# Kernel tuning notes

Measured on AMD Instinct MI355X. Metric: run time of the kernel, lower is better.

Reference implementation:

```python
import jax, jax.numpy as jnp
import numpy as np

B, T, D, H, L = 16, 1024, 1024, 1024, 2


def setup_inputs() -> dict:
    key = jax.random.key(0)
    ks = jax.random.split(key, 7)
    s_ih = float(np.sqrt(6.0 / (4 * H + D)))  # xavier_uniform bound
    s_hh = float(np.sqrt(6.0 / (4 * H + H)))
    return {
        "x": jax.random.normal(ks[0], (B, T, D), dtype=jnp.float32),
        "w_ih0": jax.random.uniform(ks[1], (4 * H, D), jnp.float32, -s_ih, s_ih),
        "w_hh0": jax.random.uniform(ks[2], (4 * H, H), jnp.float32, -s_hh, s_hh),
        "b0": jnp.zeros((4 * H,), jnp.float32),
        "w_ih1": jax.random.uniform(ks[3], (4 * H, H), jnp.float32, -s_ih, s_ih),
        "w_hh1": jax.random.uniform(ks[4], (4 * H, H), jnp.float32, -s_hh, s_hh),
        "b1": jnp.zeros((4 * H,), jnp.float32),
    }


def _cell(x, h, c, w_ih, w_hh, b):
    # gates: [B, 4H]
    gates = x @ w_ih.T + h @ w_hh.T + b
    i, f, g, o = jnp.split(gates, 4, axis=1)
    i = jnp.exp(i)            # exponential input gate (xLSTM sLSTM)
    f = jnp.exp(f)            # exponential forget gate
    g = jnp.tanh(g)
    o = jax.nn.sigmoid(o)
    c = f * c + i * g
    h = o * jnp.tanh(c)
    return h, c


def reference(x, w_ih0, w_hh0, b0, w_ih1, w_hh1, b1):
    b = x.shape[0]
    zeros = jnp.zeros((b, H), x.dtype)
    init = (zeros, zeros, zeros, zeros)  # (h0, c0, h1, c1)

    def step(carry, xt):
        h0, c0, h1, c1 = carry
        h0, c0 = _cell(xt, h0, c0, w_ih0, w_hh0, b0)
        h1, c1 = _cell(h0, h1, c1, w_ih1, w_hh1, b1)
        return (h0, c0, h1, c1), h1

    carry, ys = jax.lax.scan(step, init, jnp.swapaxes(x, 0, 1))  # time-major scan
    out = jnp.swapaxes(ys, 0, 1)  # [B, T, H]
    h0, c0, h1, c1 = carry
    return out, h0, c0, h1, c1
```

## Files before the change

kernel.cpp:

```cpp
#include <hip/hip_runtime.h>
#include <math.h>

namespace {
constexpr int Bt   = 16;
constexpr int Tt   = 1024;
constexpr int Hd   = 1024;
constexpr int NT   = 512;
constexpr int UPB  = 8;
constexpr int NROW = 32;

typedef unsigned long long u64;

__device__ __forceinline__ float sanitize_c(float v) {
  return fminf(fmaxf(v, -3.0e38f), 3.0e38f);
}

template <int CTRL>
__device__ __forceinline__ float dpp_add(float v) {
  int x = __builtin_amdgcn_update_dpp(0, __float_as_int(v), CTRL, 0xF, 0xF, true);
  return v + __int_as_float(x);
}
__device__ __forceinline__ float red8(float v) {
  v = dpp_add<0xB1>(v);
  v = dpp_add<0x4E>(v);
  v = dpp_add<0x141>(v);
  return v;
}

__device__ __forceinline__ u64 ld_h64(const float* p) {
  return __hip_atomic_load((const u64*)p, __ATOMIC_RELAXED, __HIP_MEMORY_SCOPE_AGENT);
}
__device__ __forceinline__ void st_h32(float* p, float v) {
  __hip_atomic_store(p, v, __ATOMIC_RELAXED, __HIP_MEMORY_SCOPE_AGENT);
}
}

__global__ __launch_bounds__(NT)
__attribute__((amdgpu_waves_per_eu(2, 2)))
void slstm_persist(
    const float* __restrict__ x,
    const float* __restrict__ wih0, const float* __restrict__ whh0, const float* __restrict__ b0v,
    const float* __restrict__ wih1, const float* __restrict__ whh1, const float* __restrict__ b1v,
    float* __restrict__ out, float* __restrict__ ws)
{
  __shared__ __align__(16) float in0[Bt * Hd];
  __shared__ __align__(16) float in1[Bt * Hd];
  __shared__ __align__(16) float red[64 * 17 * 4];
  __shared__ float gatel[NROW * Bt];
  __shared__ float cst[UPB * Bt];
  __shared__ float biasl[NROW];

  const int tid  = threadIdx.x;
  const int bid  = blockIdx.x;
  const int w    = tid >> 6;
  const int lane = tid & 63;
  const int kslo = lane & 7;
  const int rg   = lane >> 3;
  const int ks   = w * 8 + kslo;
  const bool isB = ks >= 32;
  const int ksl  = ks & 31;
  const int cell = bid >> 7;
  const int blk  = bid & 127;
  const int ubase = blk * UPB;

  unsigned* flags = (unsigned*)ws;
  float* h0buf = ws + 1024;
  float* h1buf = h0buf + 3 * Bt * Hd;

  const float* wmat = (cell == 0) ? (isB ? whh0 : wih0) : (isB ? whh1 : wih1);
  const float* bv   = (cell == 0) ? b0v : b1v;

  const int ro0 = ((0 + kslo) & 7) * 16;
  const int ro1 = ((1 + kslo) & 7) * 16;
  const int ro2 = ((2 + kslo) & 7) * 16;
  const int ro3 = ((3 + kslo) & 7) * 16;
  const int ro4 = ((4 + kslo) & 7) * 16;
  const int ro5 = ((5 + kslo) & 7) * 16;
  const int ro6 = ((6 + kslo) & 7) * 16;
  const int ro7 = ((7 + kslo) & 7) * 16;

  float4 w00,w01,w02,w03,w04,w05,w06,w07;
  float4 w10,w11,w12,w13,w14,w15,w16,w17;
  float4 w20,w21,w22,w23,w24,w25,w26,w27;
  float4 w30,w31,w32,w33,w34,w35,w36,w37;
#define LDW(r) { \
    const int lr = rg * 4 + r; \
    const char* wb = (const char*)(wmat + (size_t)((lr >> 3) * Hd + ubase + (lr & 7)) * Hd + ksl * 32); \
    w##r##0 = *(const float4*)(wb + ro0); w##r##1 = *(const float4*)(wb + ro1); \
    w##r##2 = *(const float4*)(wb + ro2); w##r##3 = *(const float4*)(wb + ro3); \
    w##r##4 = *(const float4*)(wb + ro4); w##r##5 = *(const float4*)(wb + ro5); \
    w##r##6 = *(const float4*)(wb + ro6); w##r##7 = *(const float4*)(wb + ro7); }
  LDW(0) LDW(1) LDW(2) LDW(3)
#undef LDW

  if (tid < NROW) biasl[tid] = bv[(tid >> 3) * Hd + ubase + (tid & 7)];
  if (tid < UPB * Bt) cst[tid] = 0.f;

  if (cell == 0) {
    #pragma unroll
    for (int p = 0; p < 8; ++p) {
      const int e = p * 2048 + tid * 4;
      const int b = e >> 10, d = e & 1023;
      *(float4*)(in0 + e) = *(const float4*)(x + (size_t)b * (Tt * Hd) + d);
    }
  }
  __syncthreads();

#define STEPC(c) { const float4 v = *(const float4*)(pb + ro##c); \
        a0 = fmaf(v.x, w0##c.x, a0); a0 = fmaf(v.y, w0##c.y, a0); \
        a0 = fmaf(v.z, w0##c.z, a0); a0 = fmaf(v.w, w0##c.w, a0); \
        a1 = fmaf(v.x, w1##c.x, a1); a1 = fmaf(v.y, w1##c.y, a1); \
        a1 = fmaf(v.z, w1##c.z, a1); a1 = fmaf(v.w, w1##c.w, a1); \
        a2 = fmaf(v.x, w2##c.x, a2); a2 = fmaf(v.y, w2##c.y, a2); \
        a2 = fmaf(v.z, w2##c.z, a2); a2 = fmaf(v.w, w2##c.w, a2); \
        a3 = fmaf(v.x, w3##c.x, a3); a3 = fmaf(v.y, w3##c.y, a3); \
        a3 = fmaf(v.z, w3##c.z, a3); a3 = fmaf(v.w, w3##c.w, a3); }
#define MATMUL(INBUF) { \
    const float* myin = (INBUF) + ksl * 32; \
    _Pragma("unroll 2") \
    for (int b = 0; b < Bt; ++b) { \
      const char* pb = (const char*)(myin + b * Hd); \
      float a0 = 0.f, a1 = 0.f, a2 = 0.f, a3 = 0.f; \
      STEPC(0) STEPC(1) STEPC(2) STEPC(3) \
      STEPC(4) STEPC(5) STEPC(6) STEPC(7) \
      a0 = red8(a0); a1 = red8(a1); a2 = red8(a2); a3 = red8(a3); \
      if (kslo == 0) \
        *(float4*)&red[((w * 8 + rg) * 17 + b) * 4] = make_float4(a0, a1, a2, a3); \
    } }

  for (int k = 0; k <= Tt + 1; ++k) {
    const bool act = (cell == 0) ? (k < Tt) : (k >= 2);

    if (w < 4) {
      if (act) { MATMUL(in0) }
    } else {
      const unsigned tgt = (unsigned)k;
      const int f = tid - 256;
      while (__hip_atomic_load(&flags[f], __ATOMIC_RELAXED, __HIP_MEMORY_SCOPE_AGENT) < tgt)
        __builtin_amdgcn_s_sleep(1);
    }
    __syncthreads();

    if (w >= 4) {
      if (act) {
        const int s = tid - 256;
        if ((cell == 0 && k == 0) || (cell == 1 && k == 2)) {
          #pragma unroll
          for (int p = 0; p < 16; ++p)
            *(float4*)(in1 + p * 1024 + s * 4) = make_float4(0.f, 0.f, 0.f, 0.f);
        } else {
          const float* src = (cell == 0) ? (h0buf + ((k - 1) % 3) * (Bt * Hd))
                                         : (h1buf + ((k - 1) & 1) * (Bt * Hd));
          #pragma unroll
          for (int p = 0; p < 16; ++p) {
            const int e = p * 1024 + s * 4;
            u64 lo = ld_h64(src + e), hi = ld_h64(src + e + 2);
            ((u64*)(in1 + e))[0] = lo;
            ((u64*)(in1 + e))[1] = hi;
          }
        }
      }
    } else {
      const int s = tid;
      if (cell == 0) {
        if (k + 1 < Tt) {
          #pragma unroll
          for (int p = 0; p < 16; ++p) {
            const int e = p * 1024 + s * 4;
            const int b = e >> 10, d = e & 1023;
            *(float4*)(in0 + e) =
                *(const float4*)(x + (size_t)b * (Tt * Hd) + (size_t)(k + 1) * Hd + d);
          }
        }
      } else if (k >= 1 && k <= Tt) {
        const float* src = h0buf + ((k - 1) % 3) * (Bt * Hd);
        #pragma unroll 8
        for (int p = 0; p < 16; ++p) {
          const int e = p * 1024 + s * 4;
          u64 lo = ld_h64(src + e), hi = ld_h64(src + e + 2);
          ((u64*)(in0 + e))[0] = lo;
          ((u64*)(in0 + e))[1] = hi;
        }
      }
    }
    __syncthreads();

    float oh = 0.f, oc = 0.f;
    if (act) {
      if (w >= 4) { MATMUL(in1) }
      __syncthreads();

      {
        const int rg2 = tid >> 6, rem = tid & 63, b2 = rem >> 2, r2 = rem & 3;
        float sgm = 0.f;
        #pragma unroll
        for (int ww = 0; ww < 8; ++ww)
          sgm += red[((ww * 8 + rg2) * 17 + b2) * 4 + r2];
        const int lr = rg2 * 4 + r2;
        gatel[lr * Bt + b2] = sgm + biasl[lr];
      }
      __syncthreads();

      if (tid < UPB * Bt) {
        const int u = tid >> 4, b2 = tid & 15;
        const float gi = gatel[(0 * UPB + u) * Bt + b2];
        const float gf = gatel[(1 * UPB + u) * Bt + b2];
        const float gg = gatel[(2 * UPB + u) * Bt + b2];
        const float go = gatel[(3 * UPB + u) * Bt + b2];
        const float ig = expf(gi);
        const float fg = expf(gf);
        const float g_ = tanhf(gg);
        const float og = 1.f / (1.f + expf(-go));
        const float cn = fg * cst[tid] + ig * g_;
        cst[tid] = cn;
        const float h = og * tanhf(cn);
        oh = h; oc = cn;
        const int j = ubase + u;
        if (cell == 0) {
          st_h32(&h0buf[(k % 3) * (Bt * Hd) + b2 * Hd + j], h);
        } else {
          st_h32(&h1buf[(k & 1) * (Bt * Hd) + b2 * Hd + j], h);
        }
      }
    }

    asm volatile("s_waitcnt vmcnt(0)" ::: "memory");
    __syncthreads();
    if (tid == 0)
      __hip_atomic_store(&flags[bid], (unsigned)(k + 1), __ATOMIC_RELAXED, __HIP_MEMORY_SCOPE_AGENT);

    if (act && tid < UPB * Bt) {
      const int u = tid >> 4, b2 = tid & 15, j = ubase + u;
      const size_t fin = (size_t)Bt * Tt * Hd;
      if (cell == 0) {
        if (k == Tt - 1) {
          out[fin + b2 * Hd + j] = oh;
          out[fin + Bt * Hd + b2 * Hd + j] = sanitize_c(oc);
        }
      } else {
        const int t = k - 2;
        out[((size_t)b2 * Tt + t) * Hd + j] = oh;
        if (t == Tt - 1) {
          out[fin + 2 * Bt * Hd + b2 * Hd + j] = oh;
          out[fin + 3 * Bt * Hd + b2 * Hd + j] = sanitize_c(oc);
        }
      }
    }
  }
  asm volatile("s_waitcnt vmcnt(0)" ::: "memory");
#undef MATMUL
#undef STEPC
}

extern "C" void kernel_launch(void* const* d_in, const int* in_sizes, int n_in,
                              void* d_out, int out_size, void* d_ws, size_t ws_size,
                              hipStream_t stream) {
  (void)hipMemsetAsync(d_ws, 0, 4096, stream);

  const float* x    = (const float*)d_in[0];
  const float* wih0 = (const float*)d_in[1];
  const float* whh0 = (const float*)d_in[2];
  const float* b0   = (const float*)d_in[3];
  const float* wih1 = (const float*)d_in[4];
  const float* whh1 = (const float*)d_in[5];
  const float* b1   = (const float*)d_in[6];

  slstm_persist<<<256, NT, 0, stream>>>(x, wih0, whh0, b0, wih1, whh1, b1,
                                        (float*)d_out, (float*)d_ws);
}
```

Measured before the change: 16.88 ms.

## Relay hidden state through per-XCD L2 mirrors with cooperative copy and XCD barrier

Each block now copies a slice of the freshly published h0/h1 buffers into a mirror buffer, using its rank within its XCD, then joins a per-XCD counter barrier. After a buffer_inv, all threads load the full hidden state from the mirror with plain float4 loads instead of many agent-scope atomic loads. The goal is to replace cross-XCD coherent reads by every block with one cooperative cross-XCD fetch per XCD, then serve the rest from the local L2. It adds an extra barrier and spin loop per timestep, and assumes exactly 32 blocks per XCD with 128 arrivals.

Result: slower. 29.66 ms (+75.7%).

```diff
diff --git a/kernel.cpp b/kernel.cpp
--- a/kernel.cpp
+++ b/kernel.cpp
@@ -8,6 +8,7 @@
 constexpr int NT   = 512;
 constexpr int UPB  = 8;
 constexpr int NROW = 32;
+constexpr int BH   = Bt * Hd;
 
 typedef unsigned long long u64;
 
@@ -32,6 +33,16 @@
 }
 __device__ __forceinline__ void st_h32(float* p, float v) {
   __hip_atomic_store(p, v, __ATOMIC_RELAXED, __HIP_MEMORY_SCOPE_AGENT);
+}
+
+__device__ __forceinline__ unsigned l2_atomic_add_ret(unsigned* p, unsigned v) {
+  unsigned old;
+  asm volatile("global_atomic_add %0, %1, %2, off sc0\n\ts_waitcnt vmcnt(0)"
+               : "=v"(old) : "v"(p), "v"(v) : "memory");
+  return old;
+}
+__device__ __forceinline__ void l2_atomic_add(unsigned* p, unsigned v) {
+  asm volatile("global_atomic_add %0, %1, off" :: "v"(p), "v"(v) : "memory");
 }
 }
 
@@ -43,12 +54,14 @@
     const float* __restrict__ wih1, const float* __restrict__ whh1, const float* __restrict__ b1v,
     float* __restrict__ out, float* __restrict__ ws)
 {
-  __shared__ __align__(16) float in0[Bt * Hd];
-  __shared__ __align__(16) float in1[Bt * Hd];
+  __shared__ __align__(16) float in0[BH];
+  __shared__ __align__(16) float in1[BH];
   __shared__ __align__(16) float red[64 * 17 * 4];
   __shared__ float gatel[NROW * Bt];
   __shared__ float cst[UPB * Bt];
   __shared__ float biasl[NROW];
+  __shared__ int lds_rank;
+  __shared__ int relayflag;
 
   const int tid  = threadIdx.x;
   const int bid  = blockIdx.x;
@@ -64,8 +77,12 @@
   const int ubase = blk * UPB;
 
   unsigned* flags = (unsigned*)ws;
+  unsigned* elect = (unsigned*)ws + 256;
+  unsigned* done  = (unsigned*)ws + 264;
   float* h0buf = ws + 1024;
-  float* h1buf = h0buf + 3 * Bt * Hd;
+  float* h1buf = h0buf + 3 * BH;
+  float* mir0  = h0buf + 5 * BH;
+  float* mir1  = h0buf + 8 * BH;
 
   const float* wmat = (cell == 0) ? (isB ? whh0 : wih0) : (isB ? whh1 : wih1);
   const float* bv   = (cell == 0) ? b0v : b1v;
@@ -93,6 +110,11 @@
   LDW(0) LDW(1) LDW(2) LDW(3)
 #undef LDW
 
+  const unsigned xcd = __builtin_amdgcn_s_getreg((31u << 11) | 20u) & 7u;
+  if (tid == 0) {
+    relayflag = 0;
+    lds_rank = (int)(l2_atomic_add_ret(elect + xcd, 1u) & 31u);
+  }
   if (tid < NROW) biasl[tid] = bv[(tid >> 3) * Hd + ubase + (tid & 7)];
   if (tid < UPB * Bt) cst[tid] = 0.f;
 
@@ -105,6 +127,7 @@
     }
   }
   __syncthreads();
+  const int rank = lds_rank;
 
 #define STEPC(c) { const float4 v = *(const float4*)(pb + ro##c); \
         a0 = fmaf(v.x, w0##c.x, a0); a0 = fmaf(v.y, w0##c.y, a0); \
@@ -130,6 +153,8 @@
 
   for (int k = 0; k <= Tt + 1; ++k) {
     const bool act = (cell == 0) ? (k < Tt) : (k >= 2);
+    const int s0 = (k + 2) % 3;
+    const int s1 = (k + 1) & 1;
 
     if (w < 4) {
       if (act) { MATMUL(in0) }
@@ -142,44 +167,83 @@
     __syncthreads();
 
     if (w >= 4) {
+      const int rt = tid - 256;
+      if (k >= 1) {
+        const int off0 = s0 * BH + rank * 512 + rt * 2;
+        u64 v = ld_h64(h0buf + off0);
+        *(u64*)(mir0 + off0) = v;
+      }
+      if (k >= 3) {
+        const int off1 = s1 * BH + rank * 512 + rt * 2;
+        u64 v = ld_h64(h1buf + off1);
+        *(u64*)(mir1 + off1) = v;
+      }
+      asm volatile("s_waitcnt vmcnt(0)" ::: "memory");
+      if (lane == 0) l2_atomic_add(done + xcd, 1u);
+    } else if (cell == 0 && k + 1 < Tt) {
+      #pragma unroll
+      for (int p = 0; p < 16; ++p) {
+        const int e = p * 1024 + tid * 4;
+        const int b = e >> 10, d = e & 1023;
+        *(float4*)(in0 + e) =
+            *(const float4*)(x + (size_t)b * (Tt * Hd) + (size_t)(k + 1) * Hd + d);
+      }
+    }
+
+    {
+      const unsigned tgt2 = 128u * (unsigned)(k + 1);
+      if (w == 4) {
+        unsigned got;
+        do {
+          unsigned o = 0;
+          if (lane == 0) o = l2_atomic_add_ret(done + xcd, 0u);
+          got = (unsigned)__builtin_amdgcn_readfirstlane((int)o);
+          if (got < tgt2) __builtin_amdgcn_s_sleep(1);
+        } while (got < tgt2);
+        if (lane == 0) *(volatile int*)&relayflag = k + 1;
+      } else {
+        while (*(volatile int*)&relayflag < k + 1) __builtin_amdgcn_s_sleep(1);
+      }
+      asm volatile("" ::: "memory");
+      asm volatile("buffer_inv" ::: "memory");
+    }
+
+    if (cell == 0) {
       if (act) {
-        const int s = tid - 256;
-        if ((cell == 0 && k == 0) || (cell == 1 && k == 2)) {
+        if (k == 0) {
           #pragma unroll
-          for (int p = 0; p < 16; ++p)
-            *(float4*)(in1 + p * 1024 + s * 4) = make_float4(0.f, 0.f, 0.f, 0.f);
+          for (int p = 0; p < 8; ++p)
+            *(float4*)(in1 + p * 2048 + tid * 4) = make_float4(0.f, 0.f, 0.f, 0.f);
         } else {
-          const float* src = (cell == 0) ? (h0buf + ((k - 1) % 3) * (Bt * Hd))
-                                         : (h1buf + ((k - 1) & 1) * (Bt * Hd));
+          const float* src = mir0 + s0 * BH;
           #pragma unroll
-          for (int p = 0; p < 16; ++p) {
-            const int e = p * 1024 + s * 4;
-            u64 lo = ld_h64(src + e), hi = ld_h64(src + e + 2);
-            ((u64*)(in1 + e))[0] = lo;
-            ((u64*)(in1 + e))[1] = hi;
+          for (int p = 0; p < 8; ++p) {
+            const int e = p * 2048 + tid * 4;
+            *(float4*)(in1 + e) = *(const float4*)(src + e);
           }
         }
       }
     } else {
-      const int s = tid;
-      if (cell == 0) {
-        if (k + 1 < Tt) {
+      if (act) {
+        if (k == 2) {
           #pragma unroll
-          for (int p = 0; p < 16; ++p) {
-            const int e = p * 1024 + s * 4;
-            const int b = e >> 10, d = e & 1023;
-            *(float4*)(in0 + e) =
-                *(const float4*)(x + (size_t)b * (Tt * Hd) + (size_t)(k + 1) * Hd + d);
+          for (int p = 0; p < 8; ++p)
+            *(float4*)(in1 + p * 2048 + tid * 4) = make_float4(0.f, 0.f, 0.f, 0.f);
+        } else {
+          const float* src = mir1 + s1 * BH;
+          #pragma unroll
+          for (int p = 0; p < 8; ++p) {
+            const int e = p * 2048 + tid * 4;
+            *(float4*)(in1 + e) = *(const float4*)(src + e);
           }
         }
-      } else if (k >= 1 && k <= Tt) {
-        const float* src = h0buf + ((k - 1) % 3) * (Bt * Hd);
-        #pragma unroll 8
-        for (int p = 0; p < 16; ++p) {
-          const int e = p * 1024 + s * 4;
-          u64 lo = ld_h64(src + e), hi = ld_h64(src + e + 2);
-          ((u64*)(in0 + e))[0] = lo;
-          ((u64*)(in0 + e))[1] = hi;
+      }
+      if (k >= 1 && k <= Tt) {
+        const float* src = mir0 + s0 * BH;
+        #pragma unroll
+        for (int p = 0; p < 8; ++p) {
+          const int e = p * 2048 + tid * 4;
+          *(float4*)(in0 + e) = *(const float4*)(src + e);
         }
       }
     }
@@ -217,9 +281,9 @@
         oh = h; oc = cn;
         const int j = ubase + u;
         if (cell == 0) {
-          st_h32(&h0buf[(k % 3) * (Bt * Hd) + b2 * Hd + j], h);
+          st_h32(&h0buf[(k % 3) * BH + b2 * Hd + j], h);
         } else {
-          st_h32(&h1buf[(k & 1) * (Bt * Hd) + b2 * Hd + j], h);
+          st_h32(&h1buf[(k & 1) * BH + b2 * Hd + j], h);
         }
       }
     }
```

## Replace per-block flag polling with hierarchical XCD-local grid barrier

Applied to the files above, without the earlier changes.

Replaces the scheme where 256 threads each poll one of 256 per-block flags with a two-level barrier: blocks arrive on a per-XCD counter, one elected leader per XCD waits for its XCD and then joins a global counter, and the other blocks wait on a per-XCD release counter. This is meant to cut polling traffic and sync latency on every timestep. It also swaps the hidden-state staging loads for inline-asm dwordx4 loads with cache-control bits, issued in batches of eight. The barrier relies on exactly 32 blocks landing on each XCD and on the workspace counters starting at zero. It adds inline-asm cache-coherence assumptions that could break correctness if they do not hold.

New measurement: 27.59 ms. +63.4%, slower.

```diff
diff --git a/kernel.cpp b/kernel.cpp
--- a/kernel.cpp
+++ b/kernel.cpp
@@ -8,6 +8,7 @@
 constexpr int NT   = 512;
 constexpr int UPB  = 8;
 constexpr int NROW = 32;
+constexpr int BH   = Bt * Hd;
 
 typedef unsigned long long u64;
 
@@ -27,12 +28,44 @@
   return v;
 }
 
-__device__ __forceinline__ u64 ld_h64(const float* p) {
-  return __hip_atomic_load((const u64*)p, __ATOMIC_RELAXED, __HIP_MEMORY_SCOPE_AGENT);
-}
 __device__ __forceinline__ void st_h32(float* p, float v) {
   __hip_atomic_store(p, v, __ATOMIC_RELAXED, __HIP_MEMORY_SCOPE_AGENT);
 }
+
+__device__ __forceinline__ unsigned l2_atomic_add_ret(unsigned* p, unsigned v) {
+  unsigned old;
+  asm volatile("global_atomic_add %0, %1, %2, off sc0\n\ts_waitcnt vmcnt(0)"
+               : "=v"(old) : "v"(p), "v"(v) : "memory");
+  return old;
+}
+__device__ __forceinline__ void l2_atomic_add(unsigned* p, unsigned v) {
+  asm volatile("global_atomic_add %0, %1, off" :: "v"(p), "v"(v) : "memory");
+}
+__device__ __forceinline__ unsigned l2_load_u32(const unsigned* p) {
+  unsigned v;
+  asm volatile("global_load_dword %0, %1, off sc0\n\ts_waitcnt vmcnt(0)"
+               : "=v"(v) : "v"(p) : "memory");
+  return v;
+}
+
+#define LD16(d, p) asm volatile("global_load_dwordx4 %0, %1, off sc1" \
+                                : "=v"(d) : "v"(p) : "memory")
+#define STAGE_SLAB(dst, src, sIdx) { \
+  _Pragma("unroll") \
+  for (int q = 0; q < 2; ++q) { \
+    float4 t0,t1,t2,t3,t4,t5,t6,t7; \
+    const int base_ = q * 8192 + (sIdx) * 4; \
+    LD16(t0, (src) + base_);        LD16(t1, (src) + base_ + 1024); \
+    LD16(t2, (src) + base_ + 2048); LD16(t3, (src) + base_ + 3072); \
+    LD16(t4, (src) + base_ + 4096); LD16(t5, (src) + base_ + 5120); \
+    LD16(t6, (src) + base_ + 6144); LD16(t7, (src) + base_ + 7168); \
+    asm volatile("s_waitcnt vmcnt(0)" ::: "memory"); \
+    __builtin_amdgcn_sched_barrier(0); \
+    *(float4*)((dst) + base_)        = t0; *(float4*)((dst) + base_ + 1024) = t1; \
+    *(float4*)((dst) + base_ + 2048) = t2; *(float4*)((dst) + base_ + 3072) = t3; \
+    *(float4*)((dst) + base_ + 4096) = t4; *(float4*)((dst) + base_ + 5120) = t5; \
+    *(float4*)((dst) + base_ + 6144) = t6; *(float4*)((dst) + base_ + 7168) = t7; \
+  } }
 }
 
 __global__ __launch_bounds__(NT)
@@ -43,12 +76,13 @@
     const float* __restrict__ wih1, const float* __restrict__ whh1, const float* __restrict__ b1v,
     float* __restrict__ out, float* __restrict__ ws)
 {
-  __shared__ __align__(16) float in0[Bt * Hd];
-  __shared__ __align__(16) float in1[Bt * Hd];
+  __shared__ __align__(16) float in0[BH];
+  __shared__ __align__(16) float in1[BH];
   __shared__ __align__(16) float red[64 * 17 * 4];
   __shared__ float gatel[NROW * Bt];
   __shared__ float cst[UPB * Bt];
   __shared__ float biasl[NROW];
+  __shared__ int lds_rank;
 
   const int tid  = threadIdx.x;
   const int bid  = blockIdx.x;
@@ -63,9 +97,10 @@
   const int blk  = bid & 127;
   const int ubase = blk * UPB;
 
-  unsigned* flags = (unsigned*)ws;
+  unsigned* cnt = (unsigned*)ws;
+  unsigned* garrive = cnt;
   float* h0buf = ws + 1024;
-  float* h1buf = h0buf + 3 * Bt * Hd;
+  float* h1buf = h0buf + 3 * BH;
 
   const float* wmat = (cell == 0) ? (isB ? whh0 : wih0) : (isB ? whh1 : wih1);
   const float* bv   = (cell == 0) ? b0v : b1v;
@@ -93,6 +128,12 @@
   LDW(0) LDW(1) LDW(2) LDW(3)
 #undef LDW
 
+  const unsigned xcd = __builtin_amdgcn_s_getreg((31u << 11) | 20u) & 7u;
+  unsigned* elect_x  = cnt + 32  + xcd * 32;
+  unsigned* arrive_x = cnt + 320 + xcd * 32;
+  unsigned* rel_x    = cnt + 608 + xcd * 32;
+  if (tid == 0)
+    lds_rank = (int)(l2_atomic_add_ret(elect_x, 1u) & 31u);
   if (tid < NROW) biasl[tid] = bv[(tid >> 3) * Hd + ubase + (tid & 7)];
   if (tid < UPB * Bt) cst[tid] = 0.f;
 
@@ -105,6 +146,7 @@
     }
   }
   __syncthreads();
+  const int rank = lds_rank;
 
 #define STEPC(c) { const float4 v = *(const float4*)(pb + ro##c); \
         a0 = fmaf(v.x, w0##c.x, a0); a0 = fmaf(v.y, w0##c.y, a0); \
@@ -130,14 +172,45 @@
 
   for (int k = 0; k <= Tt + 1; ++k) {
     const bool act = (cell == 0) ? (k < Tt) : (k >= 2);
+    const int s0 = (k + 2) % 3;
+    const int s1 = (k + 1) & 1;
 
     if (w < 4) {
       if (act) { MATMUL(in0) }
-    } else {
-      const unsigned tgt = (unsigned)k;
-      const int f = tid - 256;
-      while (__hip_atomic_load(&flags[f], __ATOMIC_RELAXED, __HIP_MEMORY_SCOPE_AGENT) < tgt)
-        __builtin_amdgcn_s_sleep(1);
+    } else if (w == 4 && k > 0) {
+      const unsigned kk = (unsigned)k;
+      if (rank == 0) {
+        unsigned a; int it = 0;
+        do {
+          unsigned o = 0;
+          if (lane == 0)
+            o = ((++it & 63) == 0) ? l2_atomic_add_ret(arrive_x, 0u)
+                                   : l2_load_u32(arrive_x);
+          a = (unsigned)__builtin_amdgcn_readfirstlane((int)o);
+          if (a < 32u * kk) __builtin_amdgcn_s_sleep(2);
+        } while (a < 32u * kk);
+        if (lane == 0)
+          __hip_atomic_fetch_add(garrive, 1u, __ATOMIC_RELAXED, __HIP_MEMORY_SCOPE_AGENT);
+        unsigned g;
+        do {
+          unsigned o = 0;
+          if (lane == 0)
+            o = __hip_atomic_load(garrive, __ATOMIC_RELAXED, __HIP_MEMORY_SCOPE_AGENT);
+          g = (unsigned)__builtin_amdgcn_readfirstlane((int)o);
+          if (g < 8u * kk) __builtin_amdgcn_s_sleep(2);
+        } while (g < 8u * kk);
+        if (lane == 0) l2_atomic_add(rel_x, 1u);
+      } else {
+        unsigned r; int it = 0;
+        do {
+          unsigned o = 0;
+          if (lane == 0)
+            o = ((++it & 63) == 0) ? l2_atomic_add_ret(rel_x, 0u)
+                                   : l2_load_u32(rel_x);
+          r = (unsigned)__builtin_amdgcn_readfirstlane((int)o);
+          if (r < kk) __builtin_amdgcn_s_sleep(2);
+        } while (r < kk);
+      }
     }
     __syncthreads();
 
@@ -149,38 +222,24 @@
           for (int p = 0; p < 16; ++p)
             *(float4*)(in1 + p * 1024 + s * 4) = make_float4(0.f, 0.f, 0.f, 0.f);
         } else {
-          const float* src = (cell == 0) ? (h0buf + ((k - 1) % 3) * (Bt * Hd))
-                                         : (h1buf + ((k - 1) & 1) * (Bt * Hd));
-          #pragma unroll
-          for (int p = 0; p < 16; ++p) {
-            const int e = p * 1024 + s * 4;
-            u64 lo = ld_h64(src + e), hi = ld_h64(src + e + 2);
-            ((u64*)(in1 + e))[0] = lo;
-            ((u64*)(in1 + e))[1] = hi;
-          }
+          const float* src = (cell == 0) ? (h0buf + s0 * BH) : (h1buf + s1 * BH);
+          STAGE_SLAB(in1, src, s)
         }
       }
     } else {
-      const int s = tid;
       if (cell == 0) {
         if (k + 1 < Tt) {
           #pragma unroll
           for (int p = 0; p < 16; ++p) {
-            const int e = p * 1024 + s * 4;
+            const int e = p * 1024 + tid * 4;
             const int b = e >> 10, d = e & 1023;
             *(float4*)(in0 + e) =
                 *(const float4*)(x + (size_t)b * (Tt * Hd) + (size_t)(k + 1) * Hd + d);
           }
         }
       } else if (k >= 1 && k <= Tt) {
-        const float* src = h0buf + ((k - 1) % 3) * (Bt * Hd);
-        #pragma unroll 8
-        for (int p = 0; p < 16; ++p) {
-          const int e = p * 1024 + s * 4;
-          u64 lo = ld_h64(src + e), hi = ld_h64(src + e + 2);
-          ((u64*)(in0 + e))[0] = lo;
-          ((u64*)(in0 + e))[1] = hi;
-        }
+        const float* src = h0buf + s0 * BH;
+        STAGE_SLAB(in0, src, tid)
       }
     }
     __syncthreads();
@@ -217,17 +276,16 @@
         oh = h; oc = cn;
         const int j = ubase + u;
         if (cell == 0) {
-          st_h32(&h0buf[(k % 3) * (Bt * Hd) + b2 * Hd + j], h);
+          st_h32(&h0buf[(k % 3) * BH + b2 * Hd + j], h);
         } else {
-          st_h32(&h1buf[(k & 1) * (Bt * Hd) + b2 * Hd + j], h);
+          st_h32(&h1buf[(k & 1) * BH + b2 * Hd + j], h);
         }
       }
     }
 
     asm volatile("s_waitcnt vmcnt(0)" ::: "memory");
     __syncthreads();
-    if (tid == 0)
-      __hip_atomic_store(&flags[bid], (unsigned)(k + 1), __ATOMIC_RELAXED, __HIP_MEMORY_SCOPE_AGENT);
+    if (tid == 0) l2_atomic_add(arrive_x, 1u);
 
     if (act && tid < UPB * Bt) {
       const int u = tid >> 4, b2 = tid & 15, j = ubase + u;
```
